# Kernel optimization log

Measured on AMD Instinct MI355X. Metric: run time of the kernel, lower is better.

The kernel has to match this reference:

```python
import jax, jax.numpy as jnp
import numpy as np

B, L, H, V, G, TGB = 128, 512, 256, 100000, 4, 128
S = 2 * L - 1  # max_sequence_tokens = 2*history_capacity - 1


def setup_inputs() -> dict:
    key = jax.random.key(0)
    ks = jax.random.split(key, 16)
    d = {}
    d['history_tokens'] = jax.random.randint(ks[0], (B, L), 0, V)
    d['history_post_tokens'] = jax.random.randint(ks[1], (B, L), 0, V)
    d['history_author_tokens'] = jax.random.randint(ks[2], (B, L), 0, V)
    d['history_action_tokens'] = jax.random.randint(ks[3], (B, L), 0, V)
    d['history_time_gap'] = jax.random.randint(ks[4], (B, L), 0, TGB + 1)
    d['history_group_ids'] = jnp.sort(jax.random.randint(ks[5], (B, L), 0, G + 1), axis=-1)
    d['lengths'] = jax.random.randint(ks[6], (B,), 0, L + 1)
    # embedding tables (padding_idx=0 rows zeroed as in nn.Embedding(padding_idx=0))
    d['token_table'] = (jax.random.normal(ks[7], (V, H)) * 0.02).at[0].set(0.0)
    d['time_table'] = (jax.random.normal(ks[8], (TGB + 1, H)) * 0.02).at[0].set(0.0)
    d['group_table'] = (jax.random.normal(ks[9], (G + 1, H)) * 0.02).at[0].set(0.0)
    d['pos_table'] = jax.random.normal(ks[10], (S, H)) * 0.02
    d['sep_token'] = jax.random.normal(ks[11], (H,)) * 0.02
    # event_projection params: LayerNorm(6H) -> Linear(6H,4H) -> SiLU -> Linear(4H,H)
    d['ln_gamma'] = jnp.ones((6 * H,), jnp.float32)
    d['ln_beta'] = jnp.zeros((6 * H,), jnp.float32)
    d['W1'] = jax.random.normal(ks[12], (6 * H, 4 * H)) * (1.0 / np.sqrt(6 * H))
    d['b1'] = jnp.zeros((4 * H,), jnp.float32)
    d['W2'] = jax.random.normal(ks[13], (4 * H, H)) * (1.0 / np.sqrt(4 * H))
    d['b2'] = jnp.zeros((H,), jnp.float32)
    return d


def _layernorm(x, g, b, eps=1e-5):
    m = x.mean(-1, keepdims=True)
    v = x.var(-1, keepdims=True)
    return (x - m) / jnp.sqrt(v + eps) * g + b


def reference(history_tokens, history_post_tokens, history_author_tokens,
              history_action_tokens, history_time_gap, history_group_ids,
              lengths, token_table, time_table, group_table, pos_table,
              sep_token, ln_gamma, ln_beta, W1, b1, W2, b2):
    # --- event embedding: 6 lookups concat -> LN -> MLP  (dropout is eval no-op)
    ev = jnp.concatenate([
        token_table[history_tokens],
        token_table[history_post_tokens],
        token_table[history_author_tokens],
        token_table[history_action_tokens],
        time_table[jnp.clip(history_time_gap, 0, TGB)],
        group_table[history_group_ids],
    ], axis=-1)  # [B, L, 6H]
    h = _layernorm(ev, ln_gamma, ln_beta)
    h = jax.nn.silu(h @ W1 + b1)
    event = h @ W2 + b2  # [B, L, H]

    # --- vectorized merge_with_sep (ragged right-aligned pack with sep at group boundaries)
    pos = jnp.arange(L)
    mask = pos[None, :] < lengths[:, None]                       # prefix validity mask
    gid_next = jnp.concatenate([history_group_ids[:, 1:], history_group_ids[:, -1:]], axis=1)
    boundary = (pos[None, :] < lengths[:, None] - 1) & (history_group_ids != gid_next)
    ex = jnp.cumsum(boundary, axis=1) - boundary                 # seps strictly before event p
    event_idx = pos[None, :] + ex                                # piece index of event p
    M = lengths + boundary.sum(axis=1)                           # total pieces per row
    shift = S - M                                                # may be negative (left-truncate)
    pos_e = shift[:, None] + event_idx
    pos_s = pos_e + 1
    valid_e = mask & (pos_e >= 0)
    valid_s = boundary & (pos_s >= 0)
    barange = jnp.arange(B)[:, None]
    buf = jnp.zeros((B, S + 1, H), event.dtype)                  # extra slot S = trash bin
    buf = buf.at[barange, jnp.where(valid_e, pos_e, S)].set(
        jnp.where(valid_e[..., None], event, 0.0))
    buf = buf.at[barange, jnp.where(valid_s, pos_s, S)].set(
        jnp.where(valid_s[..., None], sep_token, 0.0))
    merged = buf[:, :S]
    merged_mask = jnp.arange(S)[None, :] >= jnp.maximum(shift, 0)[:, None]
    merged = (merged + pos_table[None]) * merged_mask[..., None].astype(merged.dtype)
    return merged, merged_mask
```

## Files before the change

kernel.cpp:

```cpp
#include <hip/hip_runtime.h>

#define B_    128
#define L_    512
#define H_    256
#define TGB_  128
#define S_    1023
#define BL_   (B_ * L_)
#define SIXH  1536
#define FOURH 1024

typedef __bf16 bf16_t;
typedef bf16_t bf16x8 __attribute__((ext_vector_type(8)));
typedef float  f32x4  __attribute__((ext_vector_type(4)));
typedef unsigned short u16x4 __attribute__((ext_vector_type(4)));

template<int P> struct IC { static constexpr int v = P; };

__device__ __forceinline__ unsigned short f2bf(float f) {
    union { float f; unsigned u; } v; v.f = f;
    unsigned u = v.u;
    unsigned r = u + 0x7FFFu + ((u >> 16) & 1u);
    return (unsigned short)(r >> 16);
}

__device__ __forceinline__ void gload_lds16(const void* g, void* l) {
    __builtin_amdgcn_global_load_lds(
        (__attribute__((address_space(1))) void*)(void*)(g),
        (__attribute__((address_space(3))) void*)(l), 16, 0, 0);
}

__global__ __launch_bounds__(256) void transpose_bf16_kernel(
    const float* __restrict__ in, unsigned short* __restrict__ out,
    int R, int C)
{
    __shared__ float tile[32][33];
    int rb = blockIdx.x * 32, cb = blockIdx.y * 32;
    int tx = threadIdx.x & 31, ty = threadIdx.x >> 5;
    #pragma unroll
    for (int d = 0; d < 32; d += 8)
        tile[ty + d][tx] = in[(size_t)(rb + ty + d) * C + cb + tx];
    __syncthreads();
    #pragma unroll
    for (int d = 0; d < 32; d += 8)
        out[(size_t)(cb + ty + d) * R + rb + tx] = f2bf(tile[tx][ty + d]);
}

__global__ __launch_bounds__(128) void prefix_kernel(
    const int* __restrict__ lens, int* __restrict__ prefix,
    int* __restrict__ Vdev, int* __restrict__ outslot)
{
    __shared__ int sV;
    if (threadIdx.x == 0) {
        int acc = 0;
        for (int b = 0; b < B_; ++b) { prefix[b] = acc; acc += lens[b]; }
        *Vdev = acc; sV = acc;
    }
    __syncthreads();
    int V = sV;
    outslot[V + threadIdx.x] = -1;
    outslot[V + 128 + threadIdx.x] = -1;
}

__global__ __launch_bounds__(256) void embed_ln_kernel(
    const int* __restrict__ tok,  const int* __restrict__ ptok,
    const int* __restrict__ atok, const int* __restrict__ actok,
    const int* __restrict__ tgap, const int* __restrict__ gid,
    const float* __restrict__ ttab, const float* __restrict__ titab,
    const float* __restrict__ gtab, const float* __restrict__ gamma,
    const float* __restrict__ beta, const int* __restrict__ row_id,
    const int* __restrict__ Vdev, unsigned short* __restrict__ xln)
{
    int j = blockIdx.x * 4 + (threadIdx.x >> 6);
    if (j >= *Vdev) return;
    int l = threadIdx.x & 63;
    int rid = row_id[j];
    int i0 = tok[rid], i1 = ptok[rid], i2 = atok[rid], i3 = actok[rid];
    int i4 = tgap[rid]; i4 = i4 < 0 ? 0 : (i4 > TGB_ ? TGB_ : i4);
    int i5 = gid[rid];
    f32x4 v[6];
    v[0] = *(const f32x4*)(ttab  + (size_t)i0 * H_ + l * 4);
    v[1] = *(const f32x4*)(ttab  + (size_t)i1 * H_ + l * 4);
    v[2] = *(const f32x4*)(ttab  + (size_t)i2 * H_ + l * 4);
    v[3] = *(const f32x4*)(ttab  + (size_t)i3 * H_ + l * 4);
    v[4] = *(const f32x4*)(titab + (size_t)i4 * H_ + l * 4);
    v[5] = *(const f32x4*)(gtab  + (size_t)i5 * H_ + l * 4);
    float s = 0.0f, sq = 0.0f;
    #pragma unroll
    for (int k = 0; k < 6; ++k)
        #pragma unroll
        for (int c = 0; c < 4; ++c) { float f = v[k][c]; s += f; sq += f * f; }
    #pragma unroll
    for (int off = 32; off > 0; off >>= 1) {
        s  += __shfl_xor(s,  off);
        sq += __shfl_xor(sq, off);
    }
    float mean = s * (1.0f / 1536.0f);
    float var  = sq * (1.0f / 1536.0f) - mean * mean;
    float rstd = rsqrtf(var + 1e-5f);
    unsigned short* orow = xln + (size_t)j * SIXH;
    #pragma unroll
    for (int k = 0; k < 6; ++k) {
        f32x4 g = *(const f32x4*)(gamma + k * H_ + l * 4);
        f32x4 b = *(const f32x4*)(beta  + k * H_ + l * 4);
        u16x4 o;
        #pragma unroll
        for (int c = 0; c < 4; ++c)
            o[c] = f2bf((v[k][c] - mean) * rstd * g[c] + b[c]);
        *(u16x4*)(orow + k * H_ + l * 4) = o;
    }
}

template<int N, int K, int NTN, int EPI>
__global__ __launch_bounds__(512, 2) void gemm256_kernel(
    const unsigned short* __restrict__ A,
    const unsigned short* __restrict__ Bt,
    const float* __restrict__ bias,
    unsigned short* __restrict__ C,
    const int* __restrict__ outslot,
    const int* __restrict__ posC,
    const float* __restrict__ ptab,
    float* __restrict__ outF,
    const int* __restrict__ Vdev)
{
    constexpr int NT = K / 64;
    constexpr int IT = NT / 2;
    extern __shared__ __align__(16) unsigned short lds[];

    const int V = *Vdev;
    const int nact = ((V + 255) >> 8) * NTN;
    const int bid = blockIdx.x;
    if (bid >= nact) return;
    const int q = nact >> 3, r = nact & 7, x = bid & 7, o = bid >> 3;
    const int wid = (x < r ? x * (q + 1) : r * (q + 1) + (x - r) * q) + o;
    const int mt  = wid / NTN;
    const int m0  = mt * 256;
    const int n0  = (wid - mt * NTN) * 256;

    const int t = threadIdx.x;
    const int w = t >> 6, l = t & 63;
    const int wm = w >> 2, wn = w & 3;
    const int r16 = l & 15, ql = l >> 4;

    const int sg = (t & 3) ^ ((t >> 3) & 3);
    const unsigned short* As0 = A  + (size_t)(m0 + (t >> 2)) * K + sg * 8;
    const unsigned short* As1 = As0 + (size_t)128 * K;
    const unsigned short* Bs0 = Bt + (size_t)(n0 + (t >> 2)) * K + sg * 8;
    const unsigned short* Bs1 = Bs0 + (size_t)128 * K;
    unsigned short* ldsb = lds + w * 512;

    const int fr = (ql ^ ((r16 >> 1) & 3)) * 8;
    const unsigned short* la0 = lds + (wm * 128 + r16) * 32 + fr;
    const unsigned short* la1 = la0 + 32768;
    const unsigned short* lb0 = lds + 16384 + (wn * 64 + r16) * 32 + fr;
    const unsigned short* lb1 = lb0 + 32768;

    f32x4 acc[8][4];
    #pragma unroll
    for (int i = 0; i < 8; ++i)
        #pragma unroll
        for (int j = 0; j < 4; ++j) acc[i][j] = (f32x4)0.0f;

    auto ST2 = [&](const unsigned short* s0, const unsigned short* s1,
                   int dofs, int gofs) {
        gload_lds16(s0 + gofs, ldsb + dofs);
        gload_lds16(s1 + gofs, ldsb + dofs + 4096);
    };

    ST2(As0, As1, 0,     0);
    ST2(Bs0, Bs1, 16384, 0);
    ST2(As0, As1, 8192,  32);
    ST2(Bs0, Bs1, 24576, 32);
    ST2(As0, As1, 32768, 64);
    ST2(Bs0, Bs1, 49152, 64);
    asm volatile("s_waitcnt vmcnt(4)\ns_barrier" ::: "memory");

    bf16x8 bq[4];

    auto phase = [&](auto pc, bool last) {
        constexpr int P   = decltype(pc)::v;
        constexpr int BUF = P >> 2;
        constexpr int KK  = (P & 3) >> 1;
        constexpr int MH  = P & 1;
        const unsigned short* ab = (BUF ? la1 : la0) + KK * 8192 + MH * 2048;
        bf16x8 aq[4];
        if constexpr (MH == 0) {
            const unsigned short* bb = (BUF ? lb1 : lb0) + KK * 8192;
            bq[0] = *(const bf16x8*)(bb);
            bq[1] = *(const bf16x8*)(bb + 512);
            bq[2] = *(const bf16x8*)(bb + 1024);
            bq[3] = *(const bf16x8*)(bb + 1536);
        }
        aq[0] = *(const bf16x8*)(ab);
        aq[1] = *(const bf16x8*)(ab + 512);
        aq[2] = *(const bf16x8*)(ab + 1024);
        aq[3] = *(const bf16x8*)(ab + 1536);
        if constexpr (P == 0)      {            ST2(As0, As1, 40960, 96);  }
        else if constexpr (P == 1) {            ST2(Bs0, Bs1, 57344, 96);  }
        else if constexpr (P == 2) { if (!last) ST2(As0, As1, 0,     128); }
        else if constexpr (P == 3) { if (!last) ST2(Bs0, Bs1, 16384, 128); }
        else if constexpr (P == 4) { if (!last) ST2(As0, As1, 8192,  160); }
        else if constexpr (P == 5) { if (!last) ST2(Bs0, Bs1, 24576, 160); }
        else if constexpr (P == 6) { if (!last) ST2(As0, As1, 32768, 192); }
        else                       { if (!last) ST2(Bs0, Bs1, 49152, 192); }
        asm volatile("s_barrier" ::: "memory");
        __builtin_amdgcn_s_setprio(1);
        #pragma unroll
        for (int mm = 0; mm < 4; ++mm)
            #pragma unroll
            for (int nn = 0; nn < 4; ++nn)
                acc[MH * 4 + mm][nn] = __builtin_amdgcn_mfma_f32_16x16x32_bf16(
                    aq[mm], bq[nn], acc[MH * 4 + mm][nn], 0, 0, 0);
        __builtin_amdgcn_s_setprio(0);
        if constexpr (P == 3) {
            if (last) asm volatile("s_waitcnt vmcnt(0)\ns_barrier" ::: "memory");
            else      asm volatile("s_waitcnt vmcnt(4)\ns_barrier" ::: "memory");
        } else if constexpr (P == 7) {
            if (!last) asm volatile("s_waitcnt vmcnt(4)\ns_barrier" ::: "memory");
        } else {
            asm volatile("s_barrier" ::: "memory");
        }
    };

    for (int it = 0; it < IT; ++it) {
        const bool last = (it == IT - 1);
        phase(IC<0>{}, last);
        phase(IC<1>{}, last);
        phase(IC<2>{}, last);
        phase(IC<3>{}, last);
        phase(IC<4>{}, last);
        phase(IC<5>{}, last);
        phase(IC<6>{}, last);
        phase(IC<7>{}, last);
        As0 += 128; As1 += 128; Bs0 += 128; Bs1 += 128;
    }

    if constexpr (EPI == 0) {
        #pragma unroll
        for (int mi = 0; mi < 8; ++mi) {
            #pragma unroll
            for (int ni = 0; ni < 4; ++ni) {
                int col = n0 + wn * 64 + ni * 16 + r16;
                float bv = bias[col];
                #pragma unroll
                for (int j = 0; j < 4; ++j) {
                    int row = m0 + wm * 128 + mi * 16 + ql * 4 + j;
                    float v = acc[mi][ni][j] + bv;
                    v = v / (1.0f + __expf(-v));
                    C[(size_t)row * N + col] = f2bf(v);
                }
            }
        }
    } else {
        #pragma unroll
        for (int mi = 0; mi < 8; ++mi) {
            #pragma unroll
            for (int j = 0; j < 4; ++j) {
                int row = m0 + wm * 128 + mi * 16 + ql * 4 + j;
                int slot = outslot[row];
                if (slot >= 0) {
                    float* orow = outF + (size_t)slot * H_;
                    const float* prow = ptab + (size_t)posC[row] * H_;
                    #pragma unroll
                    for (int ni = 0; ni < 4; ++ni) {
                        int col = n0 + wn * 64 + ni * 16 + r16;
                        orow[col] = acc[mi][ni][j] + bias[col] + prow[col];
                    }
                }
            }
        }
    }
}

__global__ __launch_bounds__(512) void scan_scatter_kernel(
    const int* __restrict__ gid, const int* __restrict__ lengths,
    const int* __restrict__ prefix,
    int* __restrict__ idx_map, int* __restrict__ shiftb,
    int* __restrict__ row_id, int* __restrict__ outslot,
    int* __restrict__ posC)
{
    int b = blockIdx.x, i = threadIdx.x;
    int len = lengths[b];
    int g  = gid[b * L_ + i];
    int gn = (i < L_ - 1) ? gid[b * L_ + i + 1] : g;
    int bnd = (i < len - 1 && g != gn) ? 1 : 0;
    __shared__ int sc[512];
    sc[i] = bnd;
    __syncthreads();
    for (int off = 1; off < 512; off <<= 1) {
        int v = (i >= off) ? sc[i - off] : 0;
        __syncthreads();
        sc[i] += v;
        __syncthreads();
    }
    int incl  = sc[i];
    int total = sc[511];
    int ex = incl - bnd;
    int M = len + total;
    int shift = S_ - M;
    for (int s = i; s < S_; s += 512) idx_map[b * S_ + s] = -1;
    __syncthreads();
    if (i < len) {
        int p = shift + i + ex;
        idx_map[b * S_ + p] = i;
        if (bnd) idx_map[b * S_ + p + 1] = -2;
        int j = prefix[b] + i;
        row_id[j]  = b * L_ + i;
        outslot[j] = b * S_ + p;
        posC[j]    = p;
    }
    if (i == 0) shiftb[b] = shift;
}

__global__ __launch_bounds__(256) void fill_kernel(
    const int* __restrict__ idx_map, const int* __restrict__ shiftb,
    const float* __restrict__ ptab, const float* __restrict__ sep,
    float* __restrict__ out)
{
    int b = blockIdx.y;
    int s = blockIdx.x * 4 + (threadIdx.x >> 6);
    if (s >= S_) return;
    int h = (threadIdx.x & 63) * 4;
    int shift = shiftb[b];
    float* orow = out + ((size_t)b * S_ + s) * H_;
    if (s < shift) {
        *(f32x4*)(orow + h) = (f32x4)0.0f;
    } else {
        int idx = idx_map[b * S_ + s];
        if (idx == -2) {
            f32x4 pv = *(const f32x4*)(ptab + (size_t)s * H_ + h);
            f32x4 sv = *(const f32x4*)(sep + h);
            *(f32x4*)(orow + h) = pv + sv;
        }
    }
    if ((threadIdx.x & 63) == 0)
        out[(size_t)B_ * S_ * H_ + (size_t)b * S_ + s] = (s >= shift) ? 1.0f : 0.0f;
}

extern "C" void kernel_launch(void* const* d_in, const int* in_sizes, int n_in,
                              void* d_out, int out_size, void* d_ws, size_t ws_size,
                              hipStream_t stream)
{
    const int*   tok   = (const int*)d_in[0];
    const int*   ptok  = (const int*)d_in[1];
    const int*   atok  = (const int*)d_in[2];
    const int*   actok = (const int*)d_in[3];
    const int*   tgap  = (const int*)d_in[4];
    const int*   gid   = (const int*)d_in[5];
    const int*   lens  = (const int*)d_in[6];
    const float* ttab  = (const float*)d_in[7];
    const float* titab = (const float*)d_in[8];
    const float* gtab  = (const float*)d_in[9];
    const float* post  = (const float*)d_in[10];
    const float* sep   = (const float*)d_in[11];
    const float* gamma = (const float*)d_in[12];
    const float* beta  = (const float*)d_in[13];
    const float* W1    = (const float*)d_in[14];
    const float* b1    = (const float*)d_in[15];
    const float* W2    = (const float*)d_in[16];
    const float* b2    = (const float*)d_in[17];

    unsigned short* xln  = (unsigned short*)d_ws;
    unsigned short* hbuf = xln  + (size_t)BL_ * SIXH;
    unsigned short* W1T  = hbuf + (size_t)BL_ * FOURH;
    unsigned short* W2T  = W1T  + (size_t)FOURH * SIXH;
    int* idx_map = (int*)(W2T + (size_t)H_ * FOURH);
    int* shiftb  = idx_map + B_ * S_;
    int* prefix  = shiftb + B_;
    int* Vdev    = prefix + B_;
    int* row_id  = Vdev + 4;
    int* outslot = row_id + BL_;
    int* posC    = outslot + BL_ + 256;
    float* out   = (float*)d_out;

    constexpr int LDS_BYTES = 2 * 32768 * 2;
    (void)hipFuncSetAttribute((const void*)&gemm256_kernel<FOURH, SIXH, 4, 0>,
                              hipFuncAttributeMaxDynamicSharedMemorySize, LDS_BYTES);
    (void)hipFuncSetAttribute((const void*)&gemm256_kernel<H_, FOURH, 1, 2>,
                              hipFuncAttributeMaxDynamicSharedMemorySize, LDS_BYTES);

    transpose_bf16_kernel<<<dim3(SIXH / 32, FOURH / 32), 256, 0, stream>>>(W1, W1T, SIXH, FOURH);
    transpose_bf16_kernel<<<dim3(FOURH / 32, H_ / 32),   256, 0, stream>>>(W2, W2T, FOURH, H_);

    prefix_kernel<<<1, 128, 0, stream>>>(lens, prefix, Vdev, outslot);
    scan_scatter_kernel<<<B_, 512, 0, stream>>>(gid, lens, prefix, idx_map, shiftb,
                                                row_id, outslot, posC);

    embed_ln_kernel<<<BL_ / 4, 256, 0, stream>>>(tok, ptok, atok, actok, tgap, gid,
                                                 ttab, titab, gtab, gamma, beta,
                                                 row_id, Vdev, xln);

    gemm256_kernel<FOURH, SIXH, 4, 0><<<(BL_ / 256) * 4, 512, LDS_BYTES, stream>>>(
        xln, W1T, b1, hbuf, nullptr, nullptr, nullptr, nullptr, Vdev);
    gemm256_kernel<H_, FOURH, 1, 2><<<(BL_ / 256) * 1, 512, LDS_BYTES, stream>>>(
        hbuf, W2T, b2, nullptr, outslot, posC, post, out, Vdev);

    fill_kernel<<<dim3((S_ + 3) / 4, B_), 256, 0, stream>>>(idx_map, shiftb, post, sep, out);
}
```

Before: 289.9 us.

## Persistent grid for GEMM1, new 256x128 triple-buffered GEMM2, fold prefix into scan

GEMM1 becomes a persistent kernel: 512 blocks loop over the active tiles instead of launching the full worst-case grid and exiting early. GEMM2 gets its own kernel with 256x128 tiles, which doubles the block count for the narrow N=256 output, plus a 3-stage LDS pipeline with swizzled 64-wide K slices. The serial prefix_kernel is removed: each scan block computes its row prefix and the total with wave reductions, and the last block writes Vdev and the outslot padding. The aim is fewer launches, better CU fill for the second GEMM, and no single-thread serial loop, at the cost of a larger LDS footprint for GEMM2.

```diff
diff --git a/kernel.cpp b/kernel.cpp
--- a/kernel.cpp
+++ b/kernel.cpp
@@ -43,22 +43,6 @@
     #pragma unroll
     for (int d = 0; d < 32; d += 8)
         out[(size_t)(cb + ty + d) * R + rb + tx] = f2bf(tile[tx][ty + d]);
-}
-
-__global__ __launch_bounds__(128) void prefix_kernel(
-    const int* __restrict__ lens, int* __restrict__ prefix,
-    int* __restrict__ Vdev, int* __restrict__ outslot)
-{
-    __shared__ int sV;
-    if (threadIdx.x == 0) {
-        int acc = 0;
-        for (int b = 0; b < B_; ++b) { prefix[b] = acc; acc += lens[b]; }
-        *Vdev = acc; sV = acc;
-    }
-    __syncthreads();
-    int V = sV;
-    outslot[V + threadIdx.x] = -1;
-    outslot[V + 128 + threadIdx.x] = -1;
 }
 
 __global__ __launch_bounds__(256) void embed_ln_kernel(
@@ -110,131 +94,128 @@
     }
 }
 
-template<int N, int K, int NTN, int EPI>
-__global__ __launch_bounds__(512, 2) void gemm256_kernel(
+__global__ __launch_bounds__(512, 2) void gemm1_kernel(
     const unsigned short* __restrict__ A,
     const unsigned short* __restrict__ Bt,
     const float* __restrict__ bias,
     unsigned short* __restrict__ C,
-    const int* __restrict__ outslot,
-    const int* __restrict__ posC,
-    const float* __restrict__ ptab,
-    float* __restrict__ outF,
     const int* __restrict__ Vdev)
 {
+    constexpr int N = FOURH, K = SIXH, NTN = 4;
     constexpr int NT = K / 64;
     constexpr int IT = NT / 2;
     extern __shared__ __align__(16) unsigned short lds[];
 
     const int V = *Vdev;
     const int nact = ((V + 255) >> 8) * NTN;
-    const int bid = blockIdx.x;
-    if (bid >= nact) return;
-    const int q = nact >> 3, r = nact & 7, x = bid & 7, o = bid >> 3;
-    const int wid = (x < r ? x * (q + 1) : r * (q + 1) + (x - r) * q) + o;
-    const int mt  = wid / NTN;
-    const int m0  = mt * 256;
-    const int n0  = (wid - mt * NTN) * 256;
+    const int q = nact >> 3, r = nact & 7;
 
     const int t = threadIdx.x;
     const int w = t >> 6, l = t & 63;
     const int wm = w >> 2, wn = w & 3;
     const int r16 = l & 15, ql = l >> 4;
-
     const int sg = (t & 3) ^ ((t >> 3) & 3);
-    const unsigned short* As0 = A  + (size_t)(m0 + (t >> 2)) * K + sg * 8;
-    const unsigned short* As1 = As0 + (size_t)128 * K;
-    const unsigned short* Bs0 = Bt + (size_t)(n0 + (t >> 2)) * K + sg * 8;
-    const unsigned short* Bs1 = Bs0 + (size_t)128 * K;
     unsigned short* ldsb = lds + w * 512;
-
     const int fr = (ql ^ ((r16 >> 1) & 3)) * 8;
-    const unsigned short* la0 = lds + (wm * 128 + r16) * 32 + fr;
-    const unsigned short* la1 = la0 + 32768;
-    const unsigned short* lb0 = lds + 16384 + (wn * 64 + r16) * 32 + fr;
-    const unsigned short* lb1 = lb0 + 32768;
-
-    f32x4 acc[8][4];
-    #pragma unroll
-    for (int i = 0; i < 8; ++i)
-        #pragma unroll
-        for (int j = 0; j < 4; ++j) acc[i][j] = (f32x4)0.0f;
-
-    auto ST2 = [&](const unsigned short* s0, const unsigned short* s1,
-                   int dofs, int gofs) {
-        gload_lds16(s0 + gofs, ldsb + dofs);
-        gload_lds16(s1 + gofs, ldsb + dofs + 4096);
-    };
-
-    ST2(As0, As1, 0,     0);
-    ST2(Bs0, Bs1, 16384, 0);
-    ST2(As0, As1, 8192,  32);
-    ST2(Bs0, Bs1, 24576, 32);
-    ST2(As0, As1, 32768, 64);
-    ST2(Bs0, Bs1, 49152, 64);
-    asm volatile("s_waitcnt vmcnt(4)\ns_barrier" ::: "memory");
-
-    bf16x8 bq[4];
-
-    auto phase = [&](auto pc, bool last) {
-        constexpr int P   = decltype(pc)::v;
-        constexpr int BUF = P >> 2;
-        constexpr int KK  = (P & 3) >> 1;
-        constexpr int MH  = P & 1;
-        const unsigned short* ab = (BUF ? la1 : la0) + KK * 8192 + MH * 2048;
-        bf16x8 aq[4];
-        if constexpr (MH == 0) {
-            const unsigned short* bb = (BUF ? lb1 : lb0) + KK * 8192;
-            bq[0] = *(const bf16x8*)(bb);
-            bq[1] = *(const bf16x8*)(bb + 512);
-            bq[2] = *(const bf16x8*)(bb + 1024);
-            bq[3] = *(const bf16x8*)(bb + 1536);
-        }
-        aq[0] = *(const bf16x8*)(ab);
-        aq[1] = *(const bf16x8*)(ab + 512);
-        aq[2] = *(const bf16x8*)(ab + 1024);
-        aq[3] = *(const bf16x8*)(ab + 1536);
-        if constexpr (P == 0)      {            ST2(As0, As1, 40960, 96);  }
-        else if constexpr (P == 1) {            ST2(Bs0, Bs1, 57344, 96);  }
-        else if constexpr (P == 2) { if (!last) ST2(As0, As1, 0,     128); }
-        else if constexpr (P == 3) { if (!last) ST2(Bs0, Bs1, 16384, 128); }
-        else if constexpr (P == 4) { if (!last) ST2(As0, As1, 8192,  160); }
-        else if constexpr (P == 5) { if (!last) ST2(Bs0, Bs1, 24576, 160); }
-        else if constexpr (P == 6) { if (!last) ST2(As0, As1, 32768, 192); }
-        else                       { if (!last) ST2(Bs0, Bs1, 49152, 192); }
-        asm volatile("s_barrier" ::: "memory");
-        __builtin_amdgcn_s_setprio(1);
-        #pragma unroll
-        for (int mm = 0; mm < 4; ++mm)
+
+    for (int bidv = blockIdx.x; bidv < nact; bidv += 512) {
+        const int x = bidv & 7, o = bidv >> 3;
+        const int wid = (x < r ? x * (q + 1) : r * (q + 1) + (x - r) * q) + o;
+        const int mt  = wid / NTN;
+        const int m0  = mt * 256;
+        const int n0  = (wid - mt * NTN) * 256;
+
+        const unsigned short* As0 = A  + (size_t)(m0 + (t >> 2)) * K + sg * 8;
+        const unsigned short* As1 = As0 + (size_t)128 * K;
+        const unsigned short* Bs0 = Bt + (size_t)(n0 + (t >> 2)) * K + sg * 8;
+        const unsigned short* Bs1 = Bs0 + (size_t)128 * K;
+        const unsigned short* la0 = lds + (wm * 128 + r16) * 32 + fr;
+        const unsigned short* la1 = la0 + 32768;
+        const unsigned short* lb0 = lds + 16384 + (wn * 64 + r16) * 32 + fr;
+        const unsigned short* lb1 = lb0 + 32768;
+
+        f32x4 acc[8][4];
+        #pragma unroll
+        for (int i = 0; i < 8; ++i)
             #pragma unroll
-            for (int nn = 0; nn < 4; ++nn)
-                acc[MH * 4 + mm][nn] = __builtin_amdgcn_mfma_f32_16x16x32_bf16(
-                    aq[mm], bq[nn], acc[MH * 4 + mm][nn], 0, 0, 0);
-        __builtin_amdgcn_s_setprio(0);
-        if constexpr (P == 3) {
-            if (last) asm volatile("s_waitcnt vmcnt(0)\ns_barrier" ::: "memory");
-            else      asm volatile("s_waitcnt vmcnt(4)\ns_barrier" ::: "memory");
-        } else if constexpr (P == 7) {
-            if (!last) asm volatile("s_waitcnt vmcnt(4)\ns_barrier" ::: "memory");
-        } else {
+            for (int j = 0; j < 4; ++j) acc[i][j] = (f32x4)0.0f;
+
+        auto ST2 = [&](const unsigned short* s0, const unsigned short* s1,
+                       int dofs, int gofs) {
+            gload_lds16(s0 + gofs, ldsb + dofs);
+            gload_lds16(s1 + gofs, ldsb + dofs + 4096);
+        };
+
+        if (bidv != (int)blockIdx.x) __syncthreads();
+
+        ST2(As0, As1, 0,     0);
+        ST2(Bs0, Bs1, 16384, 0);
+        ST2(As0, As1, 8192,  32);
+        ST2(Bs0, Bs1, 24576, 32);
+        ST2(As0, As1, 32768, 64);
+        ST2(Bs0, Bs1, 49152, 64);
+        asm volatile("s_waitcnt vmcnt(4)\ns_barrier" ::: "memory");
+
+        bf16x8 bq[4];
+
+        auto phase = [&](auto pc, bool last) {
+            constexpr int P   = decltype(pc)::v;
+            constexpr int BUF = P >> 2;
+            constexpr int KK  = (P & 3) >> 1;
+            constexpr int MH  = P & 1;
+            const unsigned short* ab = (BUF ? la1 : la0) + KK * 8192 + MH * 2048;
+            bf16x8 aq[4];
+            if constexpr (MH == 0) {
+                const unsigned short* bb = (BUF ? lb1 : lb0) + KK * 8192;
+                bq[0] = *(const bf16x8*)(bb);
+                bq[1] = *(const bf16x8*)(bb + 512);
+                bq[2] = *(const bf16x8*)(bb + 1024);
+                bq[3] = *(const bf16x8*)(bb + 1536);
+            }
+            aq[0] = *(const bf16x8*)(ab);
+            aq[1] = *(const bf16x8*)(ab + 512);
+            aq[2] = *(const bf16x8*)(ab + 1024);
+            aq[3] = *(const bf16x8*)(ab + 1536);
+            if constexpr (P == 0)      {            ST2(As0, As1, 40960, 96);  }
+            else if constexpr (P == 1) {            ST2(Bs0, Bs1, 57344, 96);  }
+            else if constexpr (P == 2) { if (!last) ST2(As0, As1, 0,     128); }
+            else if constexpr (P == 3) { if (!last) ST2(Bs0, Bs1, 16384, 128); }
+            else if constexpr (P == 4) { if (!last) ST2(As0, As1, 8192,  160); }
+            else if constexpr (P == 5) { if (!last) ST2(Bs0, Bs1, 24576, 160); }
+            else if constexpr (P == 6) { if (!last) ST2(As0, As1, 32768, 192); }
+            else                       { if (!last) ST2(Bs0, Bs1, 49152, 192); }
             asm volatile("s_barrier" ::: "memory");
-        }
-    };
-
-    for (int it = 0; it < IT; ++it) {
-        const bool last = (it == IT - 1);
-        phase(IC<0>{}, last);
-        phase(IC<1>{}, last);
-        phase(IC<2>{}, last);
-        phase(IC<3>{}, last);
-        phase(IC<4>{}, last);
-        phase(IC<5>{}, last);
-        phase(IC<6>{}, last);
-        phase(IC<7>{}, last);
-        As0 += 128; As1 += 128; Bs0 += 128; Bs1 += 128;
-    }
-
-    if constexpr (EPI == 0) {
+            __builtin_amdgcn_s_setprio(1);
+            #pragma unroll
+            for (int mm = 0; mm < 4; ++mm)
+                #pragma unroll
+                for (int nn = 0; nn < 4; ++nn)
+                    acc[MH * 4 + mm][nn] = __builtin_amdgcn_mfma_f32_16x16x32_bf16(
+                        aq[mm], bq[nn], acc[MH * 4 + mm][nn], 0, 0, 0);
+            __builtin_amdgcn_s_setprio(0);
+            if constexpr (P == 3) {
+                if (last) asm volatile("s_waitcnt vmcnt(0)\ns_barrier" ::: "memory");
+                else      asm volatile("s_waitcnt vmcnt(4)\ns_barrier" ::: "memory");
+            } else if constexpr (P == 7) {
+                if (!last) asm volatile("s_waitcnt vmcnt(4)\ns_barrier" ::: "memory");
+            } else {
+                asm volatile("s_barrier" ::: "memory");
+            }
+        };
+
+        for (int it = 0; it < IT; ++it) {
+            const bool last = (it == IT - 1);
+            phase(IC<0>{}, last);
+            phase(IC<1>{}, last);
+            phase(IC<2>{}, last);
+            phase(IC<3>{}, last);
+            phase(IC<4>{}, last);
+            phase(IC<5>{}, last);
+            phase(IC<6>{}, last);
+            phase(IC<7>{}, last);
+            As0 += 128; As1 += 128; Bs0 += 128; Bs1 += 128;
+        }
+
         #pragma unroll
         for (int mi = 0; mi < 8; ++mi) {
             #pragma unroll
@@ -250,21 +231,126 @@
                 }
             }
         }
-    } else {
-        #pragma unroll
-        for (int mi = 0; mi < 8; ++mi) {
+    }
+}
+
+__global__ __launch_bounds__(512, 2) void gemm2_kernel(
+    const unsigned short* __restrict__ A,
+    const unsigned short* __restrict__ Bt,
+    const float* __restrict__ bias,
+    const int* __restrict__ outslot,
+    const int* __restrict__ posC,
+    const float* __restrict__ ptab,
+    float* __restrict__ outF,
+    const int* __restrict__ Vdev)
+{
+    constexpr int K = FOURH, NT = K / 64;
+    constexpr int ASLOT = 256 * 64;
+    constexpr int BSLOT = 128 * 64;
+    extern __shared__ __align__(16) unsigned short lds[];
+    unsigned short* sA = lds;
+    unsigned short* sB = lds + 3 * ASLOT;
+
+    const int V = *Vdev;
+    const int nact = ((V + 255) >> 8) * 2;
+    const int bid = blockIdx.x;
+    if (bid >= nact) return;
+    const int qd = nact >> 3, rd = nact & 7, x = bid & 7, o = bid >> 3;
+    const int wid = (x < rd ? x * (qd + 1) : rd * (qd + 1) + (x - rd) * qd) + o;
+    const int m0 = (wid >> 1) * 256;
+    const int n0 = (wid & 1) * 128;
+
+    int t = threadIdx.x;
+    int w = t >> 6, l = t & 63;
+    int srow = t >> 3;
+    int scg  = (t & 7) ^ (srow & 7);
+    const unsigned short* Ag = A  + (size_t)(m0 + srow) * K + scg * 8;
+    const unsigned short* Bg = Bt + (size_t)(n0 + srow) * K + scg * 8;
+    unsigned short* stA = sA + w * 512;
+    unsigned short* stB = sB + w * 512;
+
+    int r16 = l & 15, q = l >> 4;
+    int wm = w >> 1, wn = w & 1;
+    int xr = r16 & 7;
+    const int aoff = (wm * 64 + r16) * 64;
+    const int boff = (wn * 64 + r16) * 64;
+    const int c0 = ((0 + q) ^ xr) * 8;
+    const int c1 = ((4 + q) ^ xr) * 8;
+
+    f32x4 acc[4][4];
+    #pragma unroll
+    for (int i = 0; i < 4; ++i)
+        #pragma unroll
+        for (int j = 0; j < 4; ++j) acc[i][j] = (f32x4)0.0f;
+
+    #pragma unroll
+    for (int j = 0; j < 4; ++j) gload_lds16(Ag + (size_t)j * 64 * K, stA + j * 4096);
+    #pragma unroll
+    for (int j = 0; j < 2; ++j) gload_lds16(Bg + (size_t)j * 64 * K, stB + j * 4096);
+    #pragma unroll
+    for (int j = 0; j < 4; ++j) gload_lds16(Ag + (size_t)j * 64 * K + 64, stA + ASLOT + j * 4096);
+    #pragma unroll
+    for (int j = 0; j < 2; ++j) gload_lds16(Bg + (size_t)j * 64 * K + 64, stB + BSLOT + j * 4096);
+    asm volatile("s_waitcnt vmcnt(6)\ns_barrier" ::: "memory");
+
+    int s = 0;
+    for (int kt = 0; kt < NT; ++kt) {
+        const unsigned short* sAs = sA + s * ASLOT;
+        const unsigned short* sBs = sB + s * BSLOT;
+        int spf = s + 2; if (spf >= 3) spf -= 3;
+        const size_t gofs = (size_t)(kt + 2) * 64;
+        unsigned short* pA = stA + spf * ASLOT;
+        unsigned short* pB = stB + spf * BSLOT;
+
+        bf16x8 af[4][2];
+        #pragma unroll
+        for (int mi = 0; mi < 4; ++mi) {
+            af[mi][0] = *(const bf16x8*)(sAs + aoff + mi * 1024 + c0);
+            af[mi][1] = *(const bf16x8*)(sAs + aoff + mi * 1024 + c1);
+        }
+        #pragma unroll
+        for (int ni = 0; ni < 4; ++ni) {
+            bf16x8 b0 = *(const bf16x8*)(sBs + boff + ni * 1024 + c0);
+            bf16x8 b1 = *(const bf16x8*)(sBs + boff + ni * 1024 + c1);
+            if (kt + 2 < NT) {
+                if (ni == 0) {
+                    gload_lds16(Ag + gofs,                    pA);
+                    gload_lds16(Ag + (size_t) 64 * K + gofs,  pA + 4096);
+                } else if (ni == 1) {
+                    gload_lds16(Ag + (size_t)128 * K + gofs,  pA + 8192);
+                    gload_lds16(Ag + (size_t)192 * K + gofs,  pA + 12288);
+                } else if (ni == 2) {
+                    gload_lds16(Bg + gofs,                    pB);
+                } else {
+                    gload_lds16(Bg + (size_t) 64 * K + gofs,  pB + 4096);
+                }
+            }
+            __builtin_amdgcn_s_setprio(1);
             #pragma unroll
-            for (int j = 0; j < 4; ++j) {
-                int row = m0 + wm * 128 + mi * 16 + ql * 4 + j;
-                int slot = outslot[row];
-                if (slot >= 0) {
-                    float* orow = outF + (size_t)slot * H_;
-                    const float* prow = ptab + (size_t)posC[row] * H_;
-                    #pragma unroll
-                    for (int ni = 0; ni < 4; ++ni) {
-                        int col = n0 + wn * 64 + ni * 16 + r16;
-                        orow[col] = acc[mi][ni][j] + bias[col] + prow[col];
-                    }
+            for (int mi = 0; mi < 4; ++mi) {
+                acc[mi][ni] = __builtin_amdgcn_mfma_f32_16x16x32_bf16(af[mi][0], b0, acc[mi][ni], 0, 0, 0);
+                acc[mi][ni] = __builtin_amdgcn_mfma_f32_16x16x32_bf16(af[mi][1], b1, acc[mi][ni], 0, 0, 0);
+            }
+            __builtin_amdgcn_s_setprio(0);
+        }
+        if (kt + 2 < NT)      asm volatile("s_waitcnt vmcnt(6)\ns_barrier" ::: "memory");
+        else if (kt + 1 < NT) asm volatile("s_waitcnt vmcnt(0)\ns_barrier" ::: "memory");
+        s = (s == 2) ? 0 : s + 1;
+    }
+
+    #pragma unroll
+    for (int mi = 0; mi < 4; ++mi) {
+        #pragma unroll
+        for (int j = 0; j < 4; ++j) {
+            int row = m0 + wm * 64 + mi * 16 + q * 4 + j;
+            int slot = outslot[row];
+            if (slot >= 0) {
+                float* orow = outF + (size_t)slot * H_;
+                const float* prow = ptab + (size_t)posC[row] * H_;
+                #pragma unroll
+                for (int ni = 0; ni < 4; ++ni) {
+                    int col = n0 + wn * 64 + ni * 16 + r16;
+                    orow[col] = acc[mi][ni][j] + bias[col] + prow[col];
                 }
             }
         }
@@ -273,12 +359,25 @@
 
 __global__ __launch_bounds__(512) void scan_scatter_kernel(
     const int* __restrict__ gid, const int* __restrict__ lengths,
-    const int* __restrict__ prefix,
     int* __restrict__ idx_map, int* __restrict__ shiftb,
     int* __restrict__ row_id, int* __restrict__ outslot,
-    int* __restrict__ posC)
+    int* __restrict__ posC, int* __restrict__ Vdev)
 {
     int b = blockIdx.x, i = threadIdx.x;
+    __shared__ int slen[128];
+    __shared__ int sres[2];
+    if (i < 128) slen[i] = lengths[i];
+    __syncthreads();
+    if (i < 64) {
+        int vpart = (i < b ? slen[i] : 0) + (i + 64 < b ? slen[i + 64] : 0);
+        int vall  = slen[i] + slen[i + 64];
+        #pragma unroll
+        for (int off = 32; off > 0; off >>= 1) {
+            vpart += __shfl_xor(vpart, off);
+            vall  += __shfl_xor(vall,  off);
+        }
+        if (i == 0) { sres[0] = vpart; sres[1] = vall; }
+    }
     int len = lengths[b];
     int g  = gid[b * L_ + i];
     int gn = (i < L_ - 1) ? gid[b * L_ + i + 1] : g;
@@ -297,18 +396,23 @@
     int ex = incl - bnd;
     int M = len + total;
     int shift = S_ - M;
+    int pb = sres[0], V = sres[1];
     for (int s = i; s < S_; s += 512) idx_map[b * S_ + s] = -1;
     __syncthreads();
     if (i < len) {
         int p = shift + i + ex;
         idx_map[b * S_ + p] = i;
         if (bnd) idx_map[b * S_ + p + 1] = -2;
-        int j = prefix[b] + i;
+        int j = pb + i;
         row_id[j]  = b * L_ + i;
         outslot[j] = b * S_ + p;
         posC[j]    = p;
     }
     if (i == 0) shiftb[b] = shift;
+    if (b == B_ - 1) {
+        if (i == 0) *Vdev = V;
+        if (i < 256) outslot[V + i] = -1;
+    }
 }
 
 __global__ __launch_bounds__(256) void fill_kernel(
@@ -365,34 +469,31 @@
     unsigned short* W2T  = W1T  + (size_t)FOURH * SIXH;
     int* idx_map = (int*)(W2T + (size_t)H_ * FOURH);
     int* shiftb  = idx_map + B_ * S_;
-    int* prefix  = shiftb + B_;
-    int* Vdev    = prefix + B_;
+    int* Vdev    = shiftb + B_;
     int* row_id  = Vdev + 4;
     int* outslot = row_id + BL_;
     int* posC    = outslot + BL_ + 256;
     float* out   = (float*)d_out;
 
-    constexpr int LDS_BYTES = 2 * 32768 * 2;
-    (void)hipFuncSetAttribute((const void*)&gemm256_kernel<FOURH, SIXH, 4, 0>,
-                              hipFuncAttributeMaxDynamicSharedMemorySize, LDS_BYTES);
-    (void)hipFuncSetAttribute((const void*)&gemm256_kernel<H_, FOURH, 1, 2>,
-                              hipFuncAttributeMaxDynamicSharedMemorySize, LDS_BYTES);
+    constexpr int LDS1 = 2 * 32768 * 2;
+    constexpr int LDS2 = 3 * (256 * 64 + 128 * 64) * 2;
+    (void)hipFuncSetAttribute((const void*)&gemm1_kernel,
+                              hipFuncAttributeMaxDynamicSharedMemorySize, LDS1);
+    (void)hipFuncSetAttribute((const void*)&gemm2_kernel,
+                              hipFuncAttributeMaxDynamicSharedMemorySize, LDS2);
 
     transpose_bf16_kernel<<<dim3(SIXH / 32, FOURH / 32), 256, 0, stream>>>(W1, W1T, SIXH, FOURH);
     transpose_bf16_kernel<<<dim3(FOURH / 32, H_ / 32),   256, 0, stream>>>(W2, W2T, FOURH, H_);
 
-    prefix_kernel<<<1, 128, 0, stream>>>(lens, prefix, Vdev, outslot);
-    scan_scatter_kernel<<<B_, 512, 0, stream>>>(gid, lens, prefix, idx_map, shiftb,
-                                                row_id, outslot, posC);
+    scan_scatter_kernel<<<B_, 512, 0, stream>>>(gid, lens, idx_map, shiftb,
+                                                row_id, outslot, posC, Vdev);
 
     embed_ln_kernel<<<BL_ / 4, 256, 0, stream>>>(tok, ptok, atok, actok, tgap, gid,
                                                  ttab, titab, gtab, gamma, beta,
                                                  row_id, Vdev, xln);
 
-    gemm256_kernel<FOURH, SIXH, 4, 0><<<(BL_ / 256) * 4, 512, LDS_BYTES, stream>>>(
-        xln, W1T, b1, hbuf, nullptr, nullptr, nullptr, nullptr, Vdev);
-    gemm256_kernel<H_, FOURH, 1, 2><<<(BL_ / 256) * 1, 512, LDS_BYTES, stream>>>(
-        hbuf, W2T, b2, nullptr, outslot, posC, post, out, Vdev);
+    gemm1_kernel<<<512, 512, LDS1, stream>>>(xln, W1T, b1, hbuf, Vdev);
+    gemm2_kernel<<<512, 512, LDS2, stream>>>(hbuf, W2T, b2, outslot, posC, post, out, Vdev);
 
     fill_kernel<<<dim3((S_ + 3) / 4, B_), 256, 0, stream>>>(idx_map, shiftb, post, sep, out);
 }
```

Measured after the change: 282.4 us. -2.6%, faster.

## Switch GEMMs to persistent 128x128 tiles and fold prefix scan into scatter

Applied to the files above, without the earlier changes.

Both MLP GEMMs move from 256x256 tiles with 512 threads to 128x128 tiles with 256 threads. They now run as a persistent grid of 512 blocks that loops over the active tiles, which is meant to improve load balance and wave quantization when the count of valid rows varies. The separate single-thread prefix kernel is removed: each scan_scatter block computes its own row prefix and the total with a warp reduction, saving one launch and a serial loop. Smaller tiles lower arithmetic intensity and raise global and LDS traffic per FLOP.

```diff
diff --git a/kernel.cpp b/kernel.cpp
--- a/kernel.cpp
+++ b/kernel.cpp
@@ -43,22 +43,6 @@
     #pragma unroll
     for (int d = 0; d < 32; d += 8)
         out[(size_t)(cb + ty + d) * R + rb + tx] = f2bf(tile[tx][ty + d]);
-}
-
-__global__ __launch_bounds__(128) void prefix_kernel(
-    const int* __restrict__ lens, int* __restrict__ prefix,
-    int* __restrict__ Vdev, int* __restrict__ outslot)
-{
-    __shared__ int sV;
-    if (threadIdx.x == 0) {
-        int acc = 0;
-        for (int b = 0; b < B_; ++b) { prefix[b] = acc; acc += lens[b]; }
-        *Vdev = acc; sV = acc;
-    }
-    __syncthreads();
-    int V = sV;
-    outslot[V + threadIdx.x] = -1;
-    outslot[V + 128 + threadIdx.x] = -1;
 }
 
 __global__ __launch_bounds__(256) void embed_ln_kernel(
@@ -110,8 +94,8 @@
     }
 }
 
-template<int N, int K, int NTN, int EPI>
-__global__ __launch_bounds__(512, 2) void gemm256_kernel(
+template<int K, int NTN, int EPI>
+__global__ __launch_bounds__(256, 2) void gemm128_kernel(
     const unsigned short* __restrict__ A,
     const unsigned short* __restrict__ Bt,
     const float* __restrict__ bias,
@@ -122,148 +106,151 @@
     float* __restrict__ outF,
     const int* __restrict__ Vdev)
 {
+    constexpr int N = NTN * 128;
     constexpr int NT = K / 64;
     constexpr int IT = NT / 2;
     extern __shared__ __align__(16) unsigned short lds[];
 
     const int V = *Vdev;
-    const int nact = ((V + 255) >> 8) * NTN;
-    const int bid = blockIdx.x;
-    if (bid >= nact) return;
-    const int q = nact >> 3, r = nact & 7, x = bid & 7, o = bid >> 3;
-    const int wid = (x < r ? x * (q + 1) : r * (q + 1) + (x - r) * q) + o;
-    const int mt  = wid / NTN;
-    const int m0  = mt * 256;
-    const int n0  = (wid - mt * NTN) * 256;
+    const int nact = ((V + 127) >> 7) * NTN;
+    const int q = nact >> 3, r = nact & 7;
 
     const int t = threadIdx.x;
     const int w = t >> 6, l = t & 63;
-    const int wm = w >> 2, wn = w & 3;
+    const int wm = w >> 1, wn = w & 1;
     const int r16 = l & 15, ql = l >> 4;
-
     const int sg = (t & 3) ^ ((t >> 3) & 3);
-    const unsigned short* As0 = A  + (size_t)(m0 + (t >> 2)) * K + sg * 8;
-    const unsigned short* As1 = As0 + (size_t)128 * K;
-    const unsigned short* Bs0 = Bt + (size_t)(n0 + (t >> 2)) * K + sg * 8;
-    const unsigned short* Bs1 = Bs0 + (size_t)128 * K;
     unsigned short* ldsb = lds + w * 512;
-
     const int fr = (ql ^ ((r16 >> 1) & 3)) * 8;
-    const unsigned short* la0 = lds + (wm * 128 + r16) * 32 + fr;
-    const unsigned short* la1 = la0 + 32768;
-    const unsigned short* lb0 = lds + 16384 + (wn * 64 + r16) * 32 + fr;
-    const unsigned short* lb1 = lb0 + 32768;
-
-    f32x4 acc[8][4];
-    #pragma unroll
-    for (int i = 0; i < 8; ++i)
+
+    const unsigned short* la0 = lds + (wm * 64 + r16) * 32 + fr;
+    const unsigned short* la1 = la0 + 16384;
+    const unsigned short* lb0 = lds + 8192 + (wn * 64 + r16) * 32 + fr;
+    const unsigned short* lb1 = lb0 + 16384;
+
+    for (int bidv = blockIdx.x; bidv < nact; bidv += 512) {
+        const int x = bidv & 7, o = bidv >> 3;
+        const int wid = (x < r ? x * (q + 1) : r * (q + 1) + (x - r) * q) + o;
+        const int mt  = wid / NTN;
+        const int m0  = mt * 128;
+        const int n0  = (wid - mt * NTN) * 128;
+
+        const unsigned short* As0 = A  + (size_t)(m0 + (t >> 2)) * K + sg * 8;
+        const unsigned short* As1 = As0 + (size_t)64 * K;
+        const unsigned short* Bs0 = Bt + (size_t)(n0 + (t >> 2)) * K + sg * 8;
+        const unsigned short* Bs1 = Bs0 + (size_t)64 * K;
+
+        f32x4 acc[4][4];
         #pragma unroll
-        for (int j = 0; j < 4; ++j) acc[i][j] = (f32x4)0.0f;
-
-    auto ST2 = [&](const unsigned short* s0, const unsigned short* s1,
-                   int dofs, int gofs) {
-        gload_lds16(s0 + gofs, ldsb + dofs);
-        gload_lds16(s1 + gofs, ldsb + dofs + 4096);
-    };
-
-    ST2(As0, As1, 0,     0);
-    ST2(Bs0, Bs1, 16384, 0);
-    ST2(As0, As1, 8192,  32);
-    ST2(Bs0, Bs1, 24576, 32);
-    ST2(As0, As1, 32768, 64);
-    ST2(Bs0, Bs1, 49152, 64);
-    asm volatile("s_waitcnt vmcnt(4)\ns_barrier" ::: "memory");
-
-    bf16x8 bq[4];
-
-    auto phase = [&](auto pc, bool last) {
-        constexpr int P   = decltype(pc)::v;
-        constexpr int BUF = P >> 2;
-        constexpr int KK  = (P & 3) >> 1;
-        constexpr int MH  = P & 1;
-        const unsigned short* ab = (BUF ? la1 : la0) + KK * 8192 + MH * 2048;
-        bf16x8 aq[4];
-        if constexpr (MH == 0) {
-            const unsigned short* bb = (BUF ? lb1 : lb0) + KK * 8192;
-            bq[0] = *(const bf16x8*)(bb);
-            bq[1] = *(const bf16x8*)(bb + 512);
-            bq[2] = *(const bf16x8*)(bb + 1024);
-            bq[3] = *(const bf16x8*)(bb + 1536);
+        for (int i = 0; i < 4; ++i)
+            #pragma unroll
+            for (int j = 0; j < 4; ++j) acc[i][j] = (f32x4)0.0f;
+
+        auto ST2 = [&](const unsigned short* s0, const unsigned short* s1,
+                       int dofs, int gofs) {
+            gload_lds16(s0 + gofs, ldsb + dofs);
+            gload_lds16(s1 + gofs, ldsb + dofs + 2048);
+        };
+
+        if (bidv != (int)blockIdx.x) __syncthreads();
+
+        ST2(As0, As1, 0,     0);
+        ST2(Bs0, Bs1, 8192,  0);
+        ST2(As0, As1, 4096,  32);
+        ST2(Bs0, Bs1, 12288, 32);
+        ST2(As0, As1, 16384, 64);
+        ST2(Bs0, Bs1, 24576, 64);
+        asm volatile("s_waitcnt vmcnt(4)\ns_barrier" ::: "memory");
+
+        bf16x8 bq[4];
+
+        auto phase = [&](auto pc, bool last) {
+            constexpr int P   = decltype(pc)::v;
+            constexpr int BUF = P >> 2;
+            constexpr int KK  = (P & 3) >> 1;
+            constexpr int MH  = P & 1;
+            const unsigned short* ab = (BUF ? la1 : la0) + KK * 4096 + MH * 1024;
+            bf16x8 aq[2];
+            if constexpr (MH == 0) {
+                const unsigned short* bb = (BUF ? lb1 : lb0) + KK * 4096;
+                bq[0] = *(const bf16x8*)(bb);
+                bq[1] = *(const bf16x8*)(bb + 512);
+                bq[2] = *(const bf16x8*)(bb + 1024);
+                bq[3] = *(const bf16x8*)(bb + 1536);
+            }
+            aq[0] = *(const bf16x8*)(ab);
+            aq[1] = *(const bf16x8*)(ab + 512);
+            if constexpr (P == 0)      {            ST2(As0, As1, 20480, 96);  }
+            else if constexpr (P == 1) {            ST2(Bs0, Bs1, 28672, 96);  }
+            else if constexpr (P == 2) { if (!last) ST2(As0, As1, 0,     128); }
+            else if constexpr (P == 3) { if (!last) ST2(Bs0, Bs1, 8192,  128); }
+            else if constexpr (P == 4) { if (!last) ST2(As0, As1, 4096,  160); }
+            else if constexpr (P == 5) { if (!last) ST2(Bs0, Bs1, 12288, 160); }
+            else if constexpr (P == 6) { if (!last) ST2(As0, As1, 16384, 192); }
+            else                       { if (!last) ST2(Bs0, Bs1, 24576, 192); }
+            asm volatile("s_barrier" ::: "memory");
+            __builtin_amdgcn_s_setprio(1);
+            #pragma unroll
+            for (int mm = 0; mm < 2; ++mm)
+                #pragma unroll
+                for (int nn = 0; nn < 4; ++nn)
+                    acc[MH * 2 + mm][nn] = __builtin_amdgcn_mfma_f32_16x16x32_bf16(
+                        aq[mm], bq[nn], acc[MH * 2 + mm][nn], 0, 0, 0);
+            __builtin_amdgcn_s_setprio(0);
+            if constexpr (P == 3) {
+                if (last) asm volatile("s_waitcnt vmcnt(0)\ns_barrier" ::: "memory");
+                else      asm volatile("s_waitcnt vmcnt(4)\ns_barrier" ::: "memory");
+            } else if constexpr (P == 7) {
+                if (!last) asm volatile("s_waitcnt vmcnt(4)\ns_barrier" ::: "memory");
+            } else {
+                asm volatile("s_barrier" ::: "memory");
+            }
+        };
+
+        for (int it = 0; it < IT; ++it) {
+            const bool last = (it == IT - 1);
+            phase(IC<0>{}, last);
+            phase(IC<1>{}, last);
+            phase(IC<2>{}, last);
+            phase(IC<3>{}, last);
+            phase(IC<4>{}, last);
+            phase(IC<5>{}, last);
+            phase(IC<6>{}, last);
+            phase(IC<7>{}, last);
+            As0 += 128; As1 += 128; Bs0 += 128; Bs1 += 128;
         }
-        aq[0] = *(const bf16x8*)(ab);
-        aq[1] = *(const bf16x8*)(ab + 512);
-        aq[2] = *(const bf16x8*)(ab + 1024);
-        aq[3] = *(const bf16x8*)(ab + 1536);
-        if constexpr (P == 0)      {            ST2(As0, As1, 40960, 96);  }
-        else if constexpr (P == 1) {            ST2(Bs0, Bs1, 57344, 96);  }
-        else if constexpr (P == 2) { if (!last) ST2(As0, As1, 0,     128); }
-        else if constexpr (P == 3) { if (!last) ST2(Bs0, Bs1, 16384, 128); }
-        else if constexpr (P == 4) { if (!last) ST2(As0, As1, 8192,  160); }
-        else if constexpr (P == 5) { if (!last) ST2(Bs0, Bs1, 24576, 160); }
-        else if constexpr (P == 6) { if (!last) ST2(As0, As1, 32768, 192); }
-        else                       { if (!last) ST2(Bs0, Bs1, 49152, 192); }
-        asm volatile("s_barrier" ::: "memory");
-        __builtin_amdgcn_s_setprio(1);
-        #pragma unroll
-        for (int mm = 0; mm < 4; ++mm)
+
+        if constexpr (EPI == 0) {
             #pragma unroll
-            for (int nn = 0; nn < 4; ++nn)
-                acc[MH * 4 + mm][nn] = __builtin_amdgcn_mfma_f32_16x16x32_bf16(
-                    aq[mm], bq[nn], acc[MH * 4 + mm][nn], 0, 0, 0);
-        __builtin_amdgcn_s_setprio(0);
-        if constexpr (P == 3) {
-            if (last) asm volatile("s_waitcnt vmcnt(0)\ns_barrier" ::: "memory");
-            else      asm volatile("s_waitcnt vmcnt(4)\ns_barrier" ::: "memory");
-        } else if constexpr (P == 7) {
-            if (!last) asm volatile("s_waitcnt vmcnt(4)\ns_barrier" ::: "memory");
+            for (int mi = 0; mi < 4; ++mi) {
+                #pragma unroll
+                for (int ni = 0; ni < 4; ++ni) {
+                    int col = n0 + wn * 64 + ni * 16 + r16;
+                    float bv = bias[col];
+                    #pragma unroll
+                    for (int j = 0; j < 4; ++j) {
+                        int row = m0 + wm * 64 + mi * 16 + ql * 4 + j;
+                        float v = acc[mi][ni][j] + bv;
+                        v = v / (1.0f + __expf(-v));
+                        C[(size_t)row * N + col] = f2bf(v);
+                    }
+                }
+            }
         } else {
-            asm volatile("s_barrier" ::: "memory");
-        }
-    };
-
-    for (int it = 0; it < IT; ++it) {
-        const bool last = (it == IT - 1);
-        phase(IC<0>{}, last);
-        phase(IC<1>{}, last);
-        phase(IC<2>{}, last);
-        phase(IC<3>{}, last);
-        phase(IC<4>{}, last);
-        phase(IC<5>{}, last);
-        phase(IC<6>{}, last);
-        phase(IC<7>{}, last);
-        As0 += 128; As1 += 128; Bs0 += 128; Bs1 += 128;
-    }
-
-    if constexpr (EPI == 0) {
-        #pragma unroll
-        for (int mi = 0; mi < 8; ++mi) {
             #pragma unroll
-            for (int ni = 0; ni < 4; ++ni) {
-                int col = n0 + wn * 64 + ni * 16 + r16;
-                float bv = bias[col];
+            for (int mi = 0; mi < 4; ++mi) {
                 #pragma unroll
                 for (int j = 0; j < 4; ++j) {
-                    int row = m0 + wm * 128 + mi * 16 + ql * 4 + j;
-                    float v = acc[mi][ni][j] + bv;
-                    v = v / (1.0f + __expf(-v));
-                    C[(size_t)row * N + col] = f2bf(v);
-                }
-            }
-        }
-    } else {
-        #pragma unroll
-        for (int mi = 0; mi < 8; ++mi) {
-            #pragma unroll
-            for (int j = 0; j < 4; ++j) {
-                int row = m0 + wm * 128 + mi * 16 + ql * 4 + j;
-                int slot = outslot[row];
-                if (slot >= 0) {
-                    float* orow = outF + (size_t)slot * H_;
-                    const float* prow = ptab + (size_t)posC[row] * H_;
-                    #pragma unroll
-                    for (int ni = 0; ni < 4; ++ni) {
-                        int col = n0 + wn * 64 + ni * 16 + r16;
-                        orow[col] = acc[mi][ni][j] + bias[col] + prow[col];
+                    int row = m0 + wm * 64 + mi * 16 + ql * 4 + j;
+                    int slot = outslot[row];
+                    if (slot >= 0) {
+                        float* orow = outF + (size_t)slot * H_;
+                        const float* prow = ptab + (size_t)posC[row] * H_;
+                        #pragma unroll
+                        for (int ni = 0; ni < 4; ++ni) {
+                            int col = n0 + wn * 64 + ni * 16 + r16;
+                            orow[col] = acc[mi][ni][j] + bias[col] + prow[col];
+                        }
                     }
                 }
             }
@@ -273,12 +260,25 @@
 
 __global__ __launch_bounds__(512) void scan_scatter_kernel(
     const int* __restrict__ gid, const int* __restrict__ lengths,
-    const int* __restrict__ prefix,
     int* __restrict__ idx_map, int* __restrict__ shiftb,
     int* __restrict__ row_id, int* __restrict__ outslot,
-    int* __restrict__ posC)
+    int* __restrict__ posC, int* __restrict__ Vdev)
 {
     int b = blockIdx.x, i = threadIdx.x;
+    __shared__ int slen[128];
+    __shared__ int sres[2];
+    if (i < 128) slen[i] = lengths[i];
+    __syncthreads();
+    if (i < 64) {
+        int vpart = (i < b ? slen[i] : 0) + (i + 64 < b ? slen[i + 64] : 0);
+        int vall  = slen[i] + slen[i + 64];
+        #pragma unroll
+        for (int off = 32; off > 0; off >>= 1) {
+            vpart += __shfl_xor(vpart, off);
+            vall  += __shfl_xor(vall,  off);
+        }
+        if (i == 0) { sres[0] = vpart; sres[1] = vall; }
+    }
     int len = lengths[b];
     int g  = gid[b * L_ + i];
     int gn = (i < L_ - 1) ? gid[b * L_ + i + 1] : g;
@@ -297,18 +297,23 @@
     int ex = incl - bnd;
     int M = len + total;
     int shift = S_ - M;
+    int pb = sres[0], V = sres[1];
     for (int s = i; s < S_; s += 512) idx_map[b * S_ + s] = -1;
     __syncthreads();
     if (i < len) {
         int p = shift + i + ex;
         idx_map[b * S_ + p] = i;
         if (bnd) idx_map[b * S_ + p + 1] = -2;
-        int j = prefix[b] + i;
+        int j = pb + i;
         row_id[j]  = b * L_ + i;
         outslot[j] = b * S_ + p;
         posC[j]    = p;
     }
     if (i == 0) shiftb[b] = shift;
+    if (b == B_ - 1) {
+        if (i == 0) *Vdev = V;
+        if (i < 256) outslot[V + i] = -1;
+    }
 }
 
 __global__ __launch_bounds__(256) void fill_kernel(
@@ -365,33 +370,31 @@
     unsigned short* W2T  = W1T  + (size_t)FOURH * SIXH;
     int* idx_map = (int*)(W2T + (size_t)H_ * FOURH);
     int* shiftb  = idx_map + B_ * S_;
-    int* prefix  = shiftb + B_;
-    int* Vdev    = prefix + B_;
+    int* Vdev    = shiftb + B_;
     int* row_id  = Vdev + 4;
     int* outslot = row_id + BL_;
     int* posC    = outslot + BL_ + 256;
     float* out   = (float*)d_out;
 
-    constexpr int LDS_BYTES = 2 * 32768 * 2;
-    (void)hipFuncSetAttribute((const void*)&gemm256_kernel<FOURH, SIXH, 4, 0>,
-                              hipFuncAttributeMaxDynamicSharedMemorySize, LDS_BYTES);
-    (void)hipFuncSetAttribute((const void*)&gemm256_kernel<H_, FOURH, 1, 2>,
-                              hipFuncAttributeMaxDynamicSharedMemorySize, LDS_BYTES);
+    constexpr int LDSG = 2 * 16384 * 2;
+    (void)hipFuncSetAttribute((const void*)&gemm128_kernel<SIXH, 8, 0>,
+                              hipFuncAttributeMaxDynamicSharedMemorySize, LDSG);
+    (void)hipFuncSetAttribute((const void*)&gemm128_kernel<FOURH, 2, 2>,
+                              hipFuncAttributeMaxDynamicSharedMemorySize, LDSG);
 
     transpose_bf16_kernel<<<dim3(SIXH / 32, FOURH / 32), 256, 0, stream>>>(W1, W1T, SIXH, FOURH);
     transpose_bf16_kernel<<<dim3(FOURH / 32, H_ / 32),   256, 0, stream>>>(W2, W2T, FOURH, H_);
 
-    prefix_kernel<<<1, 128, 0, stream>>>(lens, prefix, Vdev, outslot);
-    scan_scatter_kernel<<<B_, 512, 0, stream>>>(gid, lens, prefix, idx_map, shiftb,
-                                                row_id, outslot, posC);
+    scan_scatter_kernel<<<B_, 512, 0, stream>>>(gid, lens, idx_map, shiftb,
+                                                row_id, outslot, posC, Vdev);
 
     embed_ln_kernel<<<BL_ / 4, 256, 0, stream>>>(tok, ptok, atok, actok, tgap, gid,
                                                  ttab, titab, gtab, gamma, beta,
                                                  row_id, Vdev, xln);
 
-    gemm256_kernel<FOURH, SIXH, 4, 0><<<(BL_ / 256) * 4, 512, LDS_BYTES, stream>>>(
+    gemm128_kernel<SIXH, 8, 0><<<512, 256, LDSG, stream>>>(
         xln, W1T, b1, hbuf, nullptr, nullptr, nullptr, nullptr, Vdev);
-    gemm256_kernel<H_, FOURH, 1, 2><<<(BL_ / 256) * 1, 512, LDS_BYTES, stream>>>(
+    gemm128_kernel<FOURH, 2, 2><<<512, 256, LDSG, stream>>>(
         hbuf, W2T, b2, nullptr, outslot, posC, post, out, Vdev);
 
     fill_kernel<<<dim3((S_ + 3) / 4, B_), 256, 0, stream>>>(idx_map, shiftb, post, sep, out);
```

Result: faster. 273.3 us (-5.7%).
